# Optimization experiments

Hardware: AMD Instinct MI355X
Metric: run time of the kernel (lower is better)

Reference implementation:

```python
import jax, jax.numpy as jnp
import numpy as np

DIM = 1024
HEADS = 16
HD = DIM // HEADS          # 64
SPECIAL = 8                # CLS/register tokens with full attention
GRID = 32                  # 32x32 patch grid
N = SPECIAL + GRID * GRID  # 1032
B = 8
WINDOW = 3                 # 2D sliding-window radius (7x7 box)
EPS = 1e-6


def _make_2d_mask() -> jnp.ndarray:
    """[N, N] bool mask: special tokens attend everywhere; patches use 2D local box."""
    idx = np.arange(N)
    special = (idx[:, None] < SPECIAL) | (idx[None, :] < SPECIAL)
    p = idx - SPECIAL
    r, c = p // GRID, p % GRID
    swa = (np.abs(r[:, None] - r[None, :]) <= WINDOW) & (np.abs(c[:, None] - c[None, :]) <= WINDOW)
    return jnp.asarray(special | swa)

_MASK = _make_2d_mask()


def setup_inputs() -> dict:
    key = jax.random.key(0)
    k1, k2, k3 = jax.random.split(key, 3)
    hidden_states = jax.random.normal(k1, (B, N, DIM), dtype=jnp.float32)
    qkv_w = jax.random.normal(k2, (3 * DIM, DIM), dtype=jnp.float32) * 0.02
    out_w = jax.random.normal(k3, (DIM, DIM), dtype=jnp.float32) * 0.02
    norm_q_w = jnp.ones((HD,), dtype=jnp.float32)
    norm_k_w = jnp.ones((HD,), dtype=jnp.float32)
    # Standard RoPE tables, half-dim frequencies tiled twice (rotate-half convention)
    pos = np.arange(N, dtype=np.float32)
    inv_freq = 1.0 / (10000.0 ** (np.arange(0, HD, 2, dtype=np.float32) / HD))
    ang = pos[:, None] * inv_freq[None, :]              # [N, HD/2]
    freqs_cos = jnp.asarray(np.concatenate([np.cos(ang), np.cos(ang)], axis=-1))  # [N, HD]
    freqs_sin = jnp.asarray(np.concatenate([np.sin(ang), np.sin(ang)], axis=-1))
    return dict(hidden_states=hidden_states, freqs_cos=freqs_cos, freqs_sin=freqs_sin,
                qkv_w=qkv_w, out_w=out_w, norm_q_w=norm_q_w, norm_k_w=norm_k_w)


def _rms_norm(x, w):
    return x * jax.lax.rsqrt(jnp.mean(x * x, axis=-1, keepdims=True) + EPS) * w


def _rotate_half(x):
    return jnp.concatenate([-x[..., HD // 2:], x[..., :HD // 2]], axis=-1)


def reference(hidden_states, freqs_cos, freqs_sin, qkv_w, out_w, norm_q_w, norm_k_w):
    Bn, Nn, C = hidden_states.shape
    # Fused QKV projection -> [3, B, H, N, D]
    qkv = (hidden_states @ qkv_w.T).reshape(Bn, Nn, 3, HEADS, HD).transpose(2, 0, 3, 1, 4)
    q, k, v = qkv[0], qkv[1], qkv[2]
    # per-head-dim RMSNorm on q, k
    q = _rms_norm(q, norm_q_w)
    k = _rms_norm(k, norm_k_w)
    # RoPE
    cos = freqs_cos[None, None]  # [1,1,N,D]
    sin = freqs_sin[None, None]
    q = q * cos + _rotate_half(q) * sin
    k = k * cos + _rotate_half(k) * sin
    # 2D sliding-window + global-token masked attention
    scale = 1.0 / jnp.sqrt(jnp.asarray(HD, dtype=q.dtype))
    scores = jnp.einsum('bhqd,bhkd->bhqk', q, k) * scale
    neg = jnp.asarray(jnp.finfo(scores.dtype).min, scores.dtype)
    scores = jnp.where(_MASK[None, None], scores, neg)
    probs = jax.nn.softmax(scores, axis=-1)
    attn = jnp.einsum('bhqk,bhkd->bhqd', probs, v)
    attn = attn.transpose(0, 2, 1, 3).reshape(Bn, Nn, C)
    return attn @ out_w.T
```

## Files before the change

### kernel.cpp

```cpp
#include <hip/hip_runtime.h>
#include <hip/hip_bf16.h>

typedef unsigned short ushort_t;
typedef __bf16 bf16x8 __attribute__((ext_vector_type(8)));
typedef float f32x4 __attribute__((ext_vector_type(4)));
typedef float f32x8 __attribute__((ext_vector_type(8)));

#define NTOK 1032
#define NROWS 8256
#define DIMC 1024
#define QKV_ELEMS 8454144
#define XE 8454144
#define QWE 3145728
#define OWE 1048576

__device__ __forceinline__ float bf2f(ushort_t u) {
    union { unsigned int i; float f; } v; v.i = ((unsigned int)u) << 16; return v.f;
}
__device__ __forceinline__ ushort_t f2bf(float f) {
    union { float f; unsigned int i; } v; v.f = f;
    unsigned int r = v.i + 0x7fffu + ((v.i >> 16) & 1u);
    return (ushort_t)(r >> 16);
}
__device__ __forceinline__ bf16x8 cvt8(const float* p) {
    const float4 a = *(const float4*)p;
    const float4 b = *(const float4*)(p + 4);
    bf16x8 r;
    r[0] = (__bf16)a.x; r[1] = (__bf16)a.y; r[2] = (__bf16)a.z; r[3] = (__bf16)a.w;
    r[4] = (__bf16)b.x; r[5] = (__bf16)b.y; r[6] = (__bf16)b.z; r[7] = (__bf16)b.w;
    return r;
}
__device__ __forceinline__ void load_lds16(const ushort_t* g, ushort_t* l) {
    __builtin_amdgcn_global_load_lds(
        (const __attribute__((address_space(1))) unsigned int*)g,
        (__attribute__((address_space(3))) unsigned int*)l, 16, 0, 0);
}

__global__ __launch_bounds__(256) void cvt_kernel(
    const float* __restrict__ X, const float* __restrict__ Wq,
    const float* __restrict__ Wo,
    ushort_t* __restrict__ Xb, ushort_t* __restrict__ Wqb,
    ushort_t* __restrict__ Wob)
{
    const long i8 = ((long)blockIdx.x * 256 + threadIdx.x) * 8;
    const float* src;
    ushort_t* dst;
    long off;
    if (i8 < XE)            { src = X;  dst = Xb;  off = i8; }
    else if (i8 < XE + QWE) { src = Wq; dst = Wqb; off = i8 - XE; }
    else                    { src = Wo; dst = Wob; off = i8 - XE - QWE; }
    *(bf16x8*)(dst + off) = cvt8(src + off);
}

__global__ __launch_bounds__(512, 2) void gemm256_kernel(
    const ushort_t* __restrict__ A, const ushort_t* __restrict__ W,
    ushort_t* __restrict__ QKV)
{
    __shared__ __align__(16) ushort_t A_lds[2 * 16384];
    __shared__ __align__(16) ushort_t B_lds[2 * 16384];

    const int tid  = threadIdx.x;
    const int wave = tid >> 6, lane = tid & 63;
    const int wr = wave >> 2, wc = wave & 3;
    const int fr = lane & 15, quad = lane >> 4;
    const int m0 = blockIdx.y * 256;
    const int n0 = blockIdx.x * 256;
    const bool swap = (blockIdx.x < 8);

    int aoff[4], boff[4];
    #pragma unroll
    for (int ld = 0; ld < 4; ++ld) {
        const int s   = ld * 512 + tid;
        const int row = s >> 3;
        const int kc  = ((s & 7) ^ (row & 7)) * 8;
        int ar = m0 + row; if (ar > NROWS - 1) ar = NROWS - 1;
        aoff[ld] = ar * DIMC + kc;
        boff[ld] = (n0 + row) * DIMC + kc;
    }

    const int ck0 = (quad ^ (fr & 7)) * 8;
    const int ck1 = ((quad + 4) ^ (fr & 7)) * 8;
    const int abase = (wr * 128 + fr) * 64;
    const int bbase = (wc * 64 + fr) * 64;

    f32x4 acc[8][4] = {};

#define SA(ld, t, c) load_lds16(A + aoff[ld] + (t) * 64, \
                                &A_lds[(c) * 16384 + ((ld) * 512 + tid) * 8])
#define SB(ld, t, c) load_lds16(W + boff[ld] + (t) * 64, \
                                &B_lds[(c) * 16384 + ((ld) * 512 + tid) * 8])
#define WAIT_LGKM0 asm volatile("s_waitcnt lgkmcnt(0)" ::: "memory")
#define WAIT_VM6   asm volatile("s_waitcnt vmcnt(6)"  ::: "memory")
#define WAIT_VM0   asm volatile("s_waitcnt vmcnt(0)"  ::: "memory")

    SB(0, 0, 0); SB(1, 0, 0); SB(2, 0, 0); SB(3, 0, 0);
    SA(0, 0, 0); SA(1, 0, 0); SA(2, 0, 0); SA(3, 0, 0);
    SB(0, 1, 1); SB(1, 1, 1); SB(2, 1, 1); SB(3, 1, 1);
    SA(0, 1, 1); SA(2, 1, 1);
    WAIT_VM6;
    __builtin_amdgcn_s_barrier();

    for (int t = 0; t < 16; ++t) {
        const int c = t & 1, o = c ^ 1;
        const int cb = c * 16384;
        bf16x8 bfrag[4][2];
        #pragma unroll
        for (int p = 0; p < 4; ++p) {
            bf16x8 af[2][2];
            #pragma unroll
            for (int mfi = 0; mfi < 2; ++mfi) {
                af[mfi][0] = *(const bf16x8*)&A_lds[cb + abase + (p * 2 + mfi) * 1024 + ck0];
                af[mfi][1] = *(const bf16x8*)&A_lds[cb + abase + (p * 2 + mfi) * 1024 + ck1];
            }
            if (p == 0) {
                #pragma unroll
                for (int nf = 0; nf < 4; ++nf) {
                    bfrag[nf][0] = *(const bf16x8*)&B_lds[cb + bbase + nf * 1024 + ck0];
                    bfrag[nf][1] = *(const bf16x8*)&B_lds[cb + bbase + nf * 1024 + ck1];
                }
                if (t + 1 < 16) { SA(1, t + 1, o); SA(3, t + 1, o); }
            } else if (p == 1) {
                if (t + 2 < 16) { SB(0, t + 2, c); SB(1, t + 2, c);
                                  SB(2, t + 2, c); SB(3, t + 2, c); }
            } else if (p == 2) {
                if (t + 2 < 16) { SA(0, t + 2, c); SA(2, t + 2, c); }
            }
            WAIT_LGKM0;
            if (p < 3) __builtin_amdgcn_s_barrier();
            __builtin_amdgcn_s_setprio(1);
            if (swap) {
                #pragma unroll
                for (int mfi = 0; mfi < 2; ++mfi)
                    #pragma unroll
                    for (int nf = 0; nf < 4; ++nf) {
                        acc[p * 2 + mfi][nf] = __builtin_amdgcn_mfma_f32_16x16x32_bf16(
                            bfrag[nf][0], af[mfi][0], acc[p * 2 + mfi][nf], 0, 0, 0);
                        acc[p * 2 + mfi][nf] = __builtin_amdgcn_mfma_f32_16x16x32_bf16(
                            bfrag[nf][1], af[mfi][1], acc[p * 2 + mfi][nf], 0, 0, 0);
                    }
            } else {
                #pragma unroll
                for (int mfi = 0; mfi < 2; ++mfi)
                    #pragma unroll
                    for (int nf = 0; nf < 4; ++nf) {
                        acc[p * 2 + mfi][nf] = __builtin_amdgcn_mfma_f32_16x16x32_bf16(
                            af[mfi][0], bfrag[nf][0], acc[p * 2 + mfi][nf], 0, 0, 0);
                        acc[p * 2 + mfi][nf] = __builtin_amdgcn_mfma_f32_16x16x32_bf16(
                            af[mfi][1], bfrag[nf][1], acc[p * 2 + mfi][nf], 0, 0, 0);
                    }
            }
            __builtin_amdgcn_s_setprio(0);
        }
        if (t < 14)       { WAIT_VM6; __builtin_amdgcn_s_barrier(); }
        else if (t == 14) { WAIT_VM0; __builtin_amdgcn_s_barrier(); }
    }

    const int rb = quad * 4;
    if (swap) {
        const int part   = n0 >> 10;
        const int hgbase = ((n0 & 1023) + wc * 64) >> 6;
        #pragma unroll
        for (int mf = 0; mf < 8; ++mf) {
            const int m = m0 + wr * 128 + mf * 16 + fr;
            if (m < NROWS) {
                const int bb = m / NTOK, n = m - bb * NTOK;
                ushort_t* outb = QKV + (long)part * QKV_ELEMS +
                    ((long)(bb * 16 + hgbase) * NTOK + n) * 64 + rb;
                #pragma unroll
                for (int nf = 0; nf < 4; ++nf) {
                    ushort4 pk;
                    pk.x = f2bf(acc[mf][nf][0]);
                    pk.y = f2bf(acc[mf][nf][1]);
                    pk.z = f2bf(acc[mf][nf][2]);
                    pk.w = f2bf(acc[mf][nf][3]);
                    *(ushort4*)(outb + nf * 16) = pk;
                }
            }
        }
    } else {
        const int hg = ((n0 & 1023) + wc * 64) >> 6;
        #pragma unroll
        for (int nf = 0; nf < 4; ++nf) {
            const int d = nf * 16 + fr;
            #pragma unroll
            for (int mf = 0; mf < 8; ++mf) {
                const int mb = m0 + wr * 128 + mf * 16 + rb;
                if (mb < NROWS) {
                    const int bb = mb / NTOK, n = mb - bb * NTOK;
                    ushort4 pk;
                    pk.x = f2bf(acc[mf][nf][0]);
                    pk.y = f2bf(acc[mf][nf][1]);
                    pk.z = f2bf(acc[mf][nf][2]);
                    pk.w = f2bf(acc[mf][nf][3]);
                    *(ushort4*)(QKV + 2L * QKV_ELEMS +
                        ((long)((bb * 16 + hg) * 64 + d)) * NTOK + n) = pk;
                }
            }
        }
    }
#undef SA
#undef SB
#undef WAIT_LGKM0
#undef WAIT_VM6
#undef WAIT_VM0
}

template<int MODE>
__global__ __launch_bounds__(256) void gemm_kernel(
    const ushort_t* __restrict__ A, const ushort_t* __restrict__ W,
    ushort_t* __restrict__ QKV, float* __restrict__ Out)
{
    __shared__ __align__(16) ushort_t As0[128 * 32];
    __shared__ __align__(16) ushort_t As1[128 * 32];
    __shared__ __align__(16) ushort_t Bs0[128 * 32];
    __shared__ __align__(16) ushort_t Bs1[128 * 32];
    const int tid  = threadIdx.x;
    const int wave = tid >> 6, lane = tid & 63;
    const int m0 = blockIdx.y * 128;
    const int n0 = blockIdx.x * 128;
    const bool swap = (MODE == 1) || (blockIdx.x < 16);

    f32x4 acc[4][4] = {};

    const int s0 = tid, s1 = tid + 256;
    int ar0 = m0 + (s0 >> 2); if (ar0 > NROWS - 1) ar0 = NROWS - 1;
    int ar1 = m0 + (s1 >> 2); if (ar1 > NROWS - 1) ar1 = NROWS - 1;
    const int br0 = n0 + (s0 >> 2);
    const int br1 = n0 + (s1 >> 2);
    const int kc0 = (s0 & 3) * 8, kc1 = (s1 & 3) * 8;

    const ushort_t* ga0 = A + (long)ar0 * DIMC + kc0;
    const ushort_t* ga1 = A + (long)ar1 * DIMC + kc1;
    const ushort_t* gw0 = W + (long)br0 * DIMC + kc0;
    const ushort_t* gw1 = W + (long)br1 * DIMC + kc1;
    ushort_t* la00 = &As0[s0 * 8]; ushort_t* la01 = &As1[s0 * 8];
    ushort_t* la10 = &As0[s1 * 8]; ushort_t* la11 = &As1[s1 * 8];
    ushort_t* lb00 = &Bs0[s0 * 8]; ushort_t* lb01 = &Bs1[s0 * 8];
    ushort_t* lb10 = &Bs0[s1 * 8]; ushort_t* lb11 = &Bs1[s1 * 8];

    const int wm = (wave >> 1) * 64, wn = (wave & 1) * 64;
    const int fr = lane & 15, fk = (lane >> 4) * 8;
    const int arow = (wm + fr) * 32 + fk;
    const int brow = (wn + fr) * 32 + fk;

    for (int k0 = 0; k0 < DIMC; k0 += 64) {
        load_lds16(ga0 + k0,      la00);
        load_lds16(ga0 + k0 + 32, la01);
        load_lds16(ga1 + k0,      la10);
        load_lds16(ga1 + k0 + 32, la11);
        load_lds16(gw0 + k0,      lb00);
        load_lds16(gw0 + k0 + 32, lb01);
        load_lds16(gw1 + k0,      lb10);
        load_lds16(gw1 + k0 + 32, lb11);
        __syncthreads();

        {
            bf16x8 af[4], bfr[4];
            #pragma unroll
            for (int mi = 0; mi < 4; ++mi)
                af[mi] = *(const bf16x8*)&As0[arow + mi * 16 * 32];
            #pragma unroll
            for (int ni = 0; ni < 4; ++ni)
                bfr[ni] = *(const bf16x8*)&Bs0[brow + ni * 16 * 32];
            if (swap) {
                #pragma unroll
                for (int mi = 0; mi < 4; ++mi)
                    #pragma unroll
                    for (int ni = 0; ni < 4; ++ni)
                        acc[mi][ni] = __builtin_amdgcn_mfma_f32_16x16x32_bf16(
                            bfr[ni], af[mi], acc[mi][ni], 0, 0, 0);
            } else {
                #pragma unroll
                for (int mi = 0; mi < 4; ++mi)
                    #pragma unroll
                    for (int ni = 0; ni < 4; ++ni)
                        acc[mi][ni] = __builtin_amdgcn_mfma_f32_16x16x32_bf16(
                            af[mi], bfr[ni], acc[mi][ni], 0, 0, 0);
            }
        }
        {
            bf16x8 af[4], bfr[4];
            #pragma unroll
            for (int mi = 0; mi < 4; ++mi)
                af[mi] = *(const bf16x8*)&As1[arow + mi * 16 * 32];
            #pragma unroll
            for (int ni = 0; ni < 4; ++ni)
                bfr[ni] = *(const bf16x8*)&Bs1[brow + ni * 16 * 32];
            if (swap) {
                #pragma unroll
                for (int mi = 0; mi < 4; ++mi)
                    #pragma unroll
                    for (int ni = 0; ni < 4; ++ni)
                        acc[mi][ni] = __builtin_amdgcn_mfma_f32_16x16x32_bf16(
                            bfr[ni], af[mi], acc[mi][ni], 0, 0, 0);
            } else {
                #pragma unroll
                for (int mi = 0; mi < 4; ++mi)
                    #pragma unroll
                    for (int ni = 0; ni < 4; ++ni)
                        acc[mi][ni] = __builtin_amdgcn_mfma_f32_16x16x32_bf16(
                            af[mi], bfr[ni], acc[mi][ni], 0, 0, 0);
            }
        }
        __syncthreads();
    }

    const int col = lane & 15, rb = (lane >> 4) * 4;

    if (MODE == 0 && swap) {
        const int part = n0 >> 10;
        #pragma unroll
        for (int mi = 0; mi < 4; ++mi) {
            const int m = m0 + wm + mi * 16 + col;
            if (m < NROWS) {
                const int bb = m / NTOK, n = m - bb * NTOK;
                #pragma unroll
                for (int ni = 0; ni < 4; ++ni) {
                    const int rem = (n0 & 1023) + wn + ni * 16 + rb;
                    const int hg = rem >> 6, d = rem & 63;
                    ushort4 pk;
                    pk.x = f2bf(acc[mi][ni][0]);
                    pk.y = f2bf(acc[mi][ni][1]);
                    pk.z = f2bf(acc[mi][ni][2]);
                    pk.w = f2bf(acc[mi][ni][3]);
                    *(ushort4*)(QKV + (long)part * QKV_ELEMS +
                        ((long)(bb * 16 + hg) * NTOK + n) * 64 + d) = pk;
                }
            }
        }
    } else if (MODE == 0) {
        #pragma unroll
        for (int ni = 0; ni < 4; ++ni) {
            const int o = n0 + wn + ni * 16 + col;
            const int rem = o & 1023;
            const int hg = rem >> 6, d = rem & 63;
            #pragma unroll
            for (int mi = 0; mi < 4; ++mi) {
                const int mb = m0 + wm + mi * 16 + rb;
                if (mb < NROWS) {
                    const int bb = mb / NTOK, n = mb - bb * NTOK;
                    ushort4 pk;
                    pk.x = f2bf(acc[mi][ni][0]);
                    pk.y = f2bf(acc[mi][ni][1]);
                    pk.z = f2bf(acc[mi][ni][2]);
                    pk.w = f2bf(acc[mi][ni][3]);
                    *(ushort4*)(QKV + 2L * QKV_ELEMS +
                        ((long)((bb * 16 + hg) * 64 + d)) * NTOK + n) = pk;
                }
            }
        }
    } else {
        #pragma unroll
        for (int mi = 0; mi < 4; ++mi) {
            const int m = m0 + wm + mi * 16 + col;
            if (m < NROWS) {
                #pragma unroll
                for (int ni = 0; ni < 4; ++ni) {
                    const int o = n0 + wn + ni * 16 + rb;
                    float4 pk;
                    pk.x = acc[mi][ni][0];
                    pk.y = acc[mi][ni][1];
                    pk.z = acc[mi][ni][2];
                    pk.w = acc[mi][ni][3];
                    *(float4*)(Out + (long)m * DIMC + o) = pk;
                }
            }
        }
    }
}

__global__ __launch_bounds__(256) void rope_kernel(
    ushort_t* __restrict__ Qb, ushort_t* __restrict__ Kb,
    const float* __restrict__ cosb, const float* __restrict__ sinb,
    const float* __restrict__ wq, const float* __restrict__ wk)
{
    __shared__ float wsh[64];
    const int idx = blockIdx.x * 256 + threadIdx.x;
    const int tensor = (idx >= 132096) ? 1 : 0;
    const int r = idx - tensor * 132096;
    const int n = r % NTOK;
    if (threadIdx.x < 64) wsh[threadIdx.x] = (tensor ? wk : wq)[threadIdx.x];
    __syncthreads();

    ushort_t* base = (tensor ? Kb : Qb) + (long)r * 64;
    bf16x8 xc[8];
    #pragma unroll
    for (int c = 0; c < 8; ++c) xc[c] = *(const bf16x8*)(base + c * 8);

    float ss = 0.f;
    #pragma unroll
    for (int c = 0; c < 8; ++c) {
        const f32x8 xf = __builtin_convertvector(xc[c], f32x8);
        #pragma unroll
        for (int e = 0; e < 8; ++e) ss += xf[e] * xf[e];
    }
    const float rms = rsqrtf(ss * (1.0f / 64.0f) + 1e-6f);

    const float* cosp = cosb + n * 64;
    const float* sinp = sinb + n * 64;
    #pragma unroll
    for (int c = 0; c < 8; ++c) {
        const f32x8 xf = __builtin_convertvector(xc[c], f32x8);
        const f32x8 pf = __builtin_convertvector(xc[c ^ 4], f32x8);
        const float sgn = (c < 4) ? -1.f : 1.f;
        bf16x8 o8;
        #pragma unroll
        for (int e = 0; e < 8; ++e) {
            const float xn  = xf[e] * rms * wsh[c * 8 + e];
            const float rot = sgn * pf[e] * rms * wsh[(c ^ 4) * 8 + e];
            o8[e] = (__bf16)(xn * cosp[c * 8 + e] + rot * sinp[c * 8 + e]);
        }
        *(bf16x8*)(base + c * 8) = o8;
    }
}

__global__ __launch_bounds__(256) void attn_kernel(
    const ushort_t* __restrict__ Qb, const ushort_t* __restrict__ Kb,
    const ushort_t* __restrict__ Vt, ushort_t* __restrict__ AO)
{
    __shared__ __align__(16) ushort_t KP_s[256 * 72];

    const int tid = threadIdx.x;
    const int wave = tid >> 6, lane = tid & 63;
    const int m_ = lane & 15, quad = lane >> 4;
    const int nb = wave * 64;
    const int d0 = wave * 16;

    bf16x8 ones;
    #pragma unroll
    for (int e = 0; e < 8; ++e) ones[e] = (__bf16)1.0f;

    if (blockIdx.x >= 128) {
        const int blk = blockIdx.x - 128;
        const int bh = blk & 127, qr = blk >> 7;
        const int b = bh >> 4, h = bh & 15;

        int r0 = qr - 3; if (r0 < 0) r0 = 0;
        int r1 = qr + 3; if (r1 > 31) r1 = 31;
        const int limit = 8 + (r1 - r0 + 1) * 32;

        const ushort_t* Qg  = Qb + ((long)bh * NTOK + 8 + qr * 32) * 64;
        const ushort_t* Kg  = Kb + (long)bh * NTOK * 64;
        const ushort_t* Vtg = Vt + (long)bh * 64 * NTOK;

        bf16x8 af[2][2];
        #pragma unroll
        for (int mt = 0; mt < 2; ++mt)
            #pragma unroll
            for (int ks = 0; ks < 2; ++ks)
                af[mt][ks] = *(const bf16x8*)(Qg + (mt * 16 + m_) * 64 + ks * 32 + quad * 8);

        bf16x8 bv[8];
        #pragma unroll
        for (int ks = 0; ks < 8; ++ks) {
            const int slot0 = ks * 32 + quad * 8;
            int tok0;
            if (slot0 >= limit) tok0 = 0;
            else if (slot0 < 8) tok0 = slot0;
            else tok0 = 8 + r0 * 32 + (slot0 - 8);
            bv[ks] = *(const bf16x8*)(Vtg + (long)(d0 + m_) * NTOK + tok0);
        }

        for (int c = tid; c < limit * 8; c += 256) {
            const int slot = c >> 3, c8 = (c & 7) * 8;
            const int tok = slot + (slot >= 8 ? r0 * 32 : 0);
            *(bf16x8*)&KP_s[slot * 72 + c8] = *(const bf16x8*)(Kg + (long)tok * 64 + c8);
        }
        __syncthreads();

        bf16x8 bfr[4][2];
        #pragma unroll
        for (int nt = 0; nt < 4; ++nt)
            #pragma unroll
            for (int ks = 0; ks < 2; ++ks)
                bfr[nt][ks] = *(const bf16x8*)&KP_s[(nb + nt * 16 + m_) * 72 + ks * 32 + quad * 8];

        f32x4 sacc[2][4] = {};
        #pragma unroll
        for (int mt = 0; mt < 2; ++mt)
            #pragma unroll
            for (int nt = 0; nt < 4; ++nt) {
                sacc[mt][nt] = __builtin_amdgcn_mfma_f32_16x16x32_bf16(
                    af[mt][0], bfr[nt][0], sacc[mt][nt], 0, 0, 0);
                sacc[mt][nt] = __builtin_amdgcn_mfma_f32_16x16x32_bf16(
                    af[mt][1], bfr[nt][1], sacc[mt][nt], 0, 0, 0);
            }
        __syncthreads();

        #pragma unroll
        for (int mt = 0; mt < 2; ++mt)
            #pragma unroll
            for (int nt = 0; nt < 4; ++nt) {
                const int slot = nb + nt * 16 + m_;
                const int kc = (slot - 8) & 31;
                #pragma unroll
                for (int reg = 0; reg < 4; ++reg) {
                    const int qm = mt * 16 + quad * 4 + reg;
                    const bool val = (slot < 8) ||
                        ((slot < limit) && ((unsigned)(kc - qm + 3) <= 6u));
                    const float p = val ? __expf(sacc[mt][nt][reg] * 0.125f) : 0.f;
                    KP_s[qm * 280 + slot] = f2bf(p);
                }
            }
        __syncthreads();

        f32x4 oacc[2] = {}, lacc[2] = {};
        #pragma unroll
        for (int ks = 0; ks < 8; ++ks) {
            #pragma unroll
            for (int mt = 0; mt < 2; ++mt) {
                const bf16x8 ap = *(const bf16x8*)&KP_s[(mt * 16 + m_) * 280 + ks * 32 + quad * 8];
                oacc[mt] = __builtin_amdgcn_mfma_f32_16x16x32_bf16(ap, bv[ks], oacc[mt], 0, 0, 0);
                lacc[mt] = __builtin_amdgcn_mfma_f32_16x16x32_bf16(ap, ones,   lacc[mt], 0, 0, 0);
            }
        }
        #pragma unroll
        for (int mt = 0; mt < 2; ++mt)
            #pragma unroll
            for (int reg = 0; reg < 4; ++reg) {
                const int qm = mt * 16 + quad * 4 + reg;
                const int tok = 8 + qr * 32 + qm;
                AO[((long)(b * NTOK + tok)) * DIMC + h * 64 + d0 + m_] =
                    f2bf(oacc[mt][reg] / lacc[mt][reg]);
            }
    } else {
        const int bh = blockIdx.x;
        const int b = bh >> 4, h = bh & 15;
        const ushort_t* Kg  = Kb + (long)bh * NTOK * 64;
        const ushort_t* Vtg = Vt + (long)bh * 64 * NTOK;

        bf16x8 afs[2];
        if (m_ < 8) {
            #pragma unroll
            for (int ks = 0; ks < 2; ++ks)
                afs[ks] = *(const bf16x8*)(Qb + ((long)bh * NTOK + m_) * 64 + ks * 32 + quad * 8);
        } else {
            #pragma unroll
            for (int ks = 0; ks < 2; ++ks)
                #pragma unroll
                for (int e = 0; e < 8; ++e) afs[ks][e] = (__bf16)0.f;
        }

        f32x4 oacc = {}, lacc = {};
        for (int ch = 0; ch < 5; ++ch) {
            const int tok0 = ch * 256;
            const int limit = (NTOK - tok0 < 256) ? (NTOK - tok0) : 256;

            bf16x8 bv[8];
            #pragma unroll
            for (int ks = 0; ks < 8; ++ks) {
                const int slot0 = ks * 32 + quad * 8;
                const int tok = tok0 + ((slot0 < limit) ? slot0 : 0);
                bv[ks] = *(const bf16x8*)(Vtg + (long)(d0 + m_) * NTOK + tok);
            }

            __syncthreads();
            for (int c = tid; c < limit * 8; c += 256) {
                const int slot = c >> 3, c8 = (c & 7) * 8;
                *(bf16x8*)&KP_s[slot * 72 + c8] =
                    *(const bf16x8*)(Kg + (long)(tok0 + slot) * 64 + c8);
            }
            __syncthreads();

            bf16x8 bfr[4][2];
            #pragma unroll
            for (int nt = 0; nt < 4; ++nt)
                #pragma unroll
                for (int ks = 0; ks < 2; ++ks)
                    bfr[nt][ks] = *(const bf16x8*)&KP_s[(nb + nt * 16 + m_) * 72 + ks * 32 + quad * 8];
            f32x4 sacc[4] = {};
            #pragma unroll
            for (int nt = 0; nt < 4; ++nt) {
                sacc[nt] = __builtin_amdgcn_mfma_f32_16x16x32_bf16(afs[0], bfr[nt][0], sacc[nt], 0, 0, 0);
                sacc[nt] = __builtin_amdgcn_mfma_f32_16x16x32_bf16(afs[1], bfr[nt][1], sacc[nt], 0, 0, 0);
            }
            __syncthreads();

            #pragma unroll
            for (int nt = 0; nt < 4; ++nt) {
                const int slot = nb + nt * 16 + m_;
                const bool val = (slot < limit);
                #pragma unroll
                for (int reg = 0; reg < 4; ++reg) {
                    const int qm = quad * 4 + reg;
                    const float p = val ? __expf(sacc[nt][reg] * 0.125f) : 0.f;
                    KP_s[qm * 280 + slot] = f2bf(p);
                }
            }
            __syncthreads();

            #pragma unroll
            for (int ks = 0; ks < 8; ++ks) {
                const bf16x8 ap = *(const bf16x8*)&KP_s[m_ * 280 + ks * 32 + quad * 8];
                oacc = __builtin_amdgcn_mfma_f32_16x16x32_bf16(ap, bv[ks], oacc, 0, 0, 0);
                lacc = __builtin_amdgcn_mfma_f32_16x16x32_bf16(ap, ones,   lacc, 0, 0, 0);
            }
        }

        #pragma unroll
        for (int reg = 0; reg < 4; ++reg) {
            const int qm = quad * 4 + reg;
            if (qm < 8) {
                AO[((long)(b * NTOK + qm)) * DIMC + h * 64 + d0 + m_] =
                    f2bf(oacc[reg] / lacc[reg]);
            }
        }
    }
}

extern "C" void kernel_launch(void* const* d_in, const int* in_sizes, int n_in,
                              void* d_out, int out_size, void* d_ws, size_t ws_size,
                              hipStream_t stream) {
    const float* X    = (const float*)d_in[0];
    const float* fc   = (const float*)d_in[1];
    const float* fs   = (const float*)d_in[2];
    const float* qkvw = (const float*)d_in[3];
    const float* outw = (const float*)d_in[4];
    const float* nqw  = (const float*)d_in[5];
    const float* nkw  = (const float*)d_in[6];

    ushort_t* Qb  = (ushort_t*)d_ws;
    ushort_t* Kb  = Qb + QKV_ELEMS;
    ushort_t* Vt  = Kb + QKV_ELEMS;
    ushort_t* AO  = Vt + QKV_ELEMS;
    ushort_t* Xb  = AO + QKV_ELEMS;
    ushort_t* Wqb = Xb + XE;
    ushort_t* Wob = Wqb + QWE;
    float* Out = (float*)d_out;

    cvt_kernel<<<6176, 256, 0, stream>>>(X, qkvw, outw, Xb, Wqb, Wob);
    gemm256_kernel<<<dim3(12, 33), 512, 0, stream>>>(Xb, Wqb, Qb);
    rope_kernel<<<1032, 256, 0, stream>>>(Qb, Kb, fc, fs, nqw, nkw);
    attn_kernel<<<4224, 256, 0, stream>>>(Qb, Kb, Vt, AO);
    gemm_kernel<1><<<dim3(8, 65), 256, 0, stream>>>(AO, Wob, nullptr, Out);
}
```

Measured before the change: 305.2 us.

## Use 256x256 pipelined GEMM for output projection and restructure phase barriers

Templates the 256x256 tiled, double-buffered GEMM so it also serves the output projection, writing fp32 output, and removes the older 128x128 GEMM. Separately, it rewrites the main loop into explicit phases: each phase issues LDS reads and global prefetches, then a barrier and a sched_barrier, then the MFMA block. The larger tiles give more data reuse, but the output GEMM now launches only 132 blocks, which may underfill the GPU. The extra barriers may also add synchronisation cost.

```diff
diff --git a/kernel.cpp b/kernel.cpp
--- a/kernel.cpp
+++ b/kernel.cpp
@@ -52,9 +52,10 @@
     *(bf16x8*)(dst + off) = cvt8(src + off);
 }
 
+template<int MODE>
 __global__ __launch_bounds__(512, 2) void gemm256_kernel(
     const ushort_t* __restrict__ A, const ushort_t* __restrict__ W,
-    ushort_t* __restrict__ QKV)
+    ushort_t* __restrict__ QKV, float* __restrict__ Out)
 {
     __shared__ __align__(16) ushort_t A_lds[2 * 16384];
     __shared__ __align__(16) ushort_t B_lds[2 * 16384];
@@ -65,7 +66,7 @@
     const int fr = lane & 15, quad = lane >> 4;
     const int m0 = blockIdx.y * 256;
     const int n0 = blockIdx.x * 256;
-    const bool swap = (blockIdx.x < 8);
+    const bool swap = (MODE == 1) || (blockIdx.x < 8);
 
     int aoff[4], boff[4];
     #pragma unroll
@@ -93,6 +94,37 @@
 #define WAIT_VM6   asm volatile("s_waitcnt vmcnt(6)"  ::: "memory")
 #define WAIT_VM0   asm volatile("s_waitcnt vmcnt(0)"  ::: "memory")
 
+#define READ_AF(p) \
+    af[0][0] = *(const bf16x8*)&A_lds[cb + abase + ((p) * 2 + 0) * 1024 + ck0]; \
+    af[0][1] = *(const bf16x8*)&A_lds[cb + abase + ((p) * 2 + 0) * 1024 + ck1]; \
+    af[1][0] = *(const bf16x8*)&A_lds[cb + abase + ((p) * 2 + 1) * 1024 + ck0]; \
+    af[1][1] = *(const bf16x8*)&A_lds[cb + abase + ((p) * 2 + 1) * 1024 + ck1];
+
+#define MFMA_PHASE(p) \
+    __builtin_amdgcn_s_setprio(1); \
+    if (swap) { \
+        _Pragma("unroll") \
+        for (int mfi = 0; mfi < 2; ++mfi) \
+            _Pragma("unroll") \
+            for (int nf = 0; nf < 4; ++nf) { \
+                acc[(p) * 2 + mfi][nf] = __builtin_amdgcn_mfma_f32_16x16x32_bf16( \
+                    bfrag[nf][0], af[mfi][0], acc[(p) * 2 + mfi][nf], 0, 0, 0); \
+                acc[(p) * 2 + mfi][nf] = __builtin_amdgcn_mfma_f32_16x16x32_bf16( \
+                    bfrag[nf][1], af[mfi][1], acc[(p) * 2 + mfi][nf], 0, 0, 0); \
+            } \
+    } else { \
+        _Pragma("unroll") \
+        for (int mfi = 0; mfi < 2; ++mfi) \
+            _Pragma("unroll") \
+            for (int nf = 0; nf < 4; ++nf) { \
+                acc[(p) * 2 + mfi][nf] = __builtin_amdgcn_mfma_f32_16x16x32_bf16( \
+                    af[mfi][0], bfrag[nf][0], acc[(p) * 2 + mfi][nf], 0, 0, 0); \
+                acc[(p) * 2 + mfi][nf] = __builtin_amdgcn_mfma_f32_16x16x32_bf16( \
+                    af[mfi][1], bfrag[nf][1], acc[(p) * 2 + mfi][nf], 0, 0, 0); \
+            } \
+    } \
+    __builtin_amdgcn_s_setprio(0);
+
     SB(0, 0, 0); SB(1, 0, 0); SB(2, 0, 0); SB(3, 0, 0);
     SA(0, 0, 0); SA(1, 0, 0); SA(2, 0, 0); SA(3, 0, 0);
     SB(0, 1, 1); SB(1, 1, 1); SB(2, 1, 1); SB(3, 1, 1);
@@ -104,59 +136,62 @@
         const int c = t & 1, o = c ^ 1;
         const int cb = c * 16384;
         bf16x8 bfrag[4][2];
-        #pragma unroll
-        for (int p = 0; p < 4; ++p) {
-            bf16x8 af[2][2];
-            #pragma unroll
-            for (int mfi = 0; mfi < 2; ++mfi) {
-                af[mfi][0] = *(const bf16x8*)&A_lds[cb + abase + (p * 2 + mfi) * 1024 + ck0];
-                af[mfi][1] = *(const bf16x8*)&A_lds[cb + abase + (p * 2 + mfi) * 1024 + ck1];
-            }
-            if (p == 0) {
-                #pragma unroll
-                for (int nf = 0; nf < 4; ++nf) {
-                    bfrag[nf][0] = *(const bf16x8*)&B_lds[cb + bbase + nf * 1024 + ck0];
-                    bfrag[nf][1] = *(const bf16x8*)&B_lds[cb + bbase + nf * 1024 + ck1];
-                }
-                if (t + 1 < 16) { SA(1, t + 1, o); SA(3, t + 1, o); }
-            } else if (p == 1) {
-                if (t + 2 < 16) { SB(0, t + 2, c); SB(1, t + 2, c);
-                                  SB(2, t + 2, c); SB(3, t + 2, c); }
-            } else if (p == 2) {
-                if (t + 2 < 16) { SA(0, t + 2, c); SA(2, t + 2, c); }
-            }
-            WAIT_LGKM0;
-            if (p < 3) __builtin_amdgcn_s_barrier();
-            __builtin_amdgcn_s_setprio(1);
-            if (swap) {
-                #pragma unroll
-                for (int mfi = 0; mfi < 2; ++mfi)
-                    #pragma unroll
-                    for (int nf = 0; nf < 4; ++nf) {
-                        acc[p * 2 + mfi][nf] = __builtin_amdgcn_mfma_f32_16x16x32_bf16(
-                            bfrag[nf][0], af[mfi][0], acc[p * 2 + mfi][nf], 0, 0, 0);
-                        acc[p * 2 + mfi][nf] = __builtin_amdgcn_mfma_f32_16x16x32_bf16(
-                            bfrag[nf][1], af[mfi][1], acc[p * 2 + mfi][nf], 0, 0, 0);
-                    }
-            } else {
-                #pragma unroll
-                for (int mfi = 0; mfi < 2; ++mfi)
-                    #pragma unroll
-                    for (int nf = 0; nf < 4; ++nf) {
-                        acc[p * 2 + mfi][nf] = __builtin_amdgcn_mfma_f32_16x16x32_bf16(
-                            af[mfi][0], bfrag[nf][0], acc[p * 2 + mfi][nf], 0, 0, 0);
-                        acc[p * 2 + mfi][nf] = __builtin_amdgcn_mfma_f32_16x16x32_bf16(
-                            af[mfi][1], bfrag[nf][1], acc[p * 2 + mfi][nf], 0, 0, 0);
-                    }
-            }
-            __builtin_amdgcn_s_setprio(0);
-        }
+        bf16x8 af[2][2];
+
+        #pragma unroll
+        for (int nf = 0; nf < 4; ++nf) {
+            bfrag[nf][0] = *(const bf16x8*)&B_lds[cb + bbase + nf * 1024 + ck0];
+            bfrag[nf][1] = *(const bf16x8*)&B_lds[cb + bbase + nf * 1024 + ck1];
+        }
+        READ_AF(0);
+        if (t < 15) { SA(1, t + 1, o); SA(3, t + 1, o); }
+        __builtin_amdgcn_s_barrier();
+        WAIT_LGKM0; __builtin_amdgcn_sched_barrier(0);
+        MFMA_PHASE(0);
+        __builtin_amdgcn_s_barrier();
+
+        READ_AF(1);
+        if (t < 14) { SB(0, t + 2, c); SB(1, t + 2, c);
+                      SB(2, t + 2, c); SB(3, t + 2, c); }
+        __builtin_amdgcn_s_barrier();
+        WAIT_LGKM0; __builtin_amdgcn_sched_barrier(0);
+        MFMA_PHASE(1);
+        __builtin_amdgcn_s_barrier();
+
+        READ_AF(2);
+        if (t < 14) { SA(0, t + 2, c); SA(2, t + 2, c); }
+        __builtin_amdgcn_s_barrier();
+        WAIT_LGKM0; __builtin_amdgcn_sched_barrier(0);
+        MFMA_PHASE(2);
+
+        READ_AF(3);
+        __builtin_amdgcn_s_barrier();
+        WAIT_LGKM0; __builtin_amdgcn_sched_barrier(0);
+        MFMA_PHASE(3);
+
         if (t < 14)       { WAIT_VM6; __builtin_amdgcn_s_barrier(); }
         else if (t == 14) { WAIT_VM0; __builtin_amdgcn_s_barrier(); }
     }
 
     const int rb = quad * 4;
-    if (swap) {
+    if (MODE == 1) {
+        #pragma unroll
+        for (int mf = 0; mf < 8; ++mf) {
+            const int m = m0 + wr * 128 + mf * 16 + fr;
+            if (m < NROWS) {
+                #pragma unroll
+                for (int nf = 0; nf < 4; ++nf) {
+                    const int o_ = n0 + wc * 64 + nf * 16 + rb;
+                    float4 pk;
+                    pk.x = acc[mf][nf][0];
+                    pk.y = acc[mf][nf][1];
+                    pk.z = acc[mf][nf][2];
+                    pk.w = acc[mf][nf][3];
+                    *(float4*)(Out + (long)m * DIMC + o_) = pk;
+                }
+            }
+        }
+    } else if (swap) {
         const int part   = n0 >> 10;
         const int hgbase = ((n0 & 1023) + wc * 64) >> 6;
         #pragma unroll
@@ -203,170 +238,8 @@
 #undef WAIT_LGKM0
 #undef WAIT_VM6
 #undef WAIT_VM0
-}
-
-template<int MODE>
-__global__ __launch_bounds__(256) void gemm_kernel(
-    const ushort_t* __restrict__ A, const ushort_t* __restrict__ W,
-    ushort_t* __restrict__ QKV, float* __restrict__ Out)
-{
-    __shared__ __align__(16) ushort_t As0[128 * 32];
-    __shared__ __align__(16) ushort_t As1[128 * 32];
-    __shared__ __align__(16) ushort_t Bs0[128 * 32];
-    __shared__ __align__(16) ushort_t Bs1[128 * 32];
-    const int tid  = threadIdx.x;
-    const int wave = tid >> 6, lane = tid & 63;
-    const int m0 = blockIdx.y * 128;
-    const int n0 = blockIdx.x * 128;
-    const bool swap = (MODE == 1) || (blockIdx.x < 16);
-
-    f32x4 acc[4][4] = {};
-
-    const int s0 = tid, s1 = tid + 256;
-    int ar0 = m0 + (s0 >> 2); if (ar0 > NROWS - 1) ar0 = NROWS - 1;
-    int ar1 = m0 + (s1 >> 2); if (ar1 > NROWS - 1) ar1 = NROWS - 1;
-    const int br0 = n0 + (s0 >> 2);
-    const int br1 = n0 + (s1 >> 2);
-    const int kc0 = (s0 & 3) * 8, kc1 = (s1 & 3) * 8;
-
-    const ushort_t* ga0 = A + (long)ar0 * DIMC + kc0;
-    const ushort_t* ga1 = A + (long)ar1 * DIMC + kc1;
-    const ushort_t* gw0 = W + (long)br0 * DIMC + kc0;
-    const ushort_t* gw1 = W + (long)br1 * DIMC + kc1;
-    ushort_t* la00 = &As0[s0 * 8]; ushort_t* la01 = &As1[s0 * 8];
-    ushort_t* la10 = &As0[s1 * 8]; ushort_t* la11 = &As1[s1 * 8];
-    ushort_t* lb00 = &Bs0[s0 * 8]; ushort_t* lb01 = &Bs1[s0 * 8];
-    ushort_t* lb10 = &Bs0[s1 * 8]; ushort_t* lb11 = &Bs1[s1 * 8];
-
-    const int wm = (wave >> 1) * 64, wn = (wave & 1) * 64;
-    const int fr = lane & 15, fk = (lane >> 4) * 8;
-    const int arow = (wm + fr) * 32 + fk;
-    const int brow = (wn + fr) * 32 + fk;
-
-    for (int k0 = 0; k0 < DIMC; k0 += 64) {
-        load_lds16(ga0 + k0,      la00);
-        load_lds16(ga0 + k0 + 32, la01);
-        load_lds16(ga1 + k0,      la10);
-        load_lds16(ga1 + k0 + 32, la11);
-        load_lds16(gw0 + k0,      lb00);
-        load_lds16(gw0 + k0 + 32, lb01);
-        load_lds16(gw1 + k0,      lb10);
-        load_lds16(gw1 + k0 + 32, lb11);
-        __syncthreads();
-
-        {
-            bf16x8 af[4], bfr[4];
-            #pragma unroll
-            for (int mi = 0; mi < 4; ++mi)
-                af[mi] = *(const bf16x8*)&As0[arow + mi * 16 * 32];
-            #pragma unroll
-            for (int ni = 0; ni < 4; ++ni)
-                bfr[ni] = *(const bf16x8*)&Bs0[brow + ni * 16 * 32];
-            if (swap) {
-                #pragma unroll
-                for (int mi = 0; mi < 4; ++mi)
-                    #pragma unroll
-                    for (int ni = 0; ni < 4; ++ni)
-                        acc[mi][ni] = __builtin_amdgcn_mfma_f32_16x16x32_bf16(
-                            bfr[ni], af[mi], acc[mi][ni], 0, 0, 0);
-            } else {
-                #pragma unroll
-                for (int mi = 0; mi < 4; ++mi)
-                    #pragma unroll
-                    for (int ni = 0; ni < 4; ++ni)
-                        acc[mi][ni] = __builtin_amdgcn_mfma_f32_16x16x32_bf16(
-                            af[mi], bfr[ni], acc[mi][ni], 0, 0, 0);
-            }
-        }
-        {
-            bf16x8 af[4], bfr[4];
-            #pragma unroll
-            for (int mi = 0; mi < 4; ++mi)
-                af[mi] = *(const bf16x8*)&As1[arow + mi * 16 * 32];
-            #pragma unroll
-            for (int ni = 0; ni < 4; ++ni)
-                bfr[ni] = *(const bf16x8*)&Bs1[brow + ni * 16 * 32];
-            if (swap) {
-                #pragma unroll
-                for (int mi = 0; mi < 4; ++mi)
-                    #pragma unroll
-                    for (int ni = 0; ni < 4; ++ni)
-                        acc[mi][ni] = __builtin_amdgcn_mfma_f32_16x16x32_bf16(
-                            bfr[ni], af[mi], acc[mi][ni], 0, 0, 0);
-            } else {
-                #pragma unroll
-                for (int mi = 0; mi < 4; ++mi)
-                    #pragma unroll
-                    for (int ni = 0; ni < 4; ++ni)
-                        acc[mi][ni] = __builtin_amdgcn_mfma_f32_16x16x32_bf16(
-                            af[mi], bfr[ni], acc[mi][ni], 0, 0, 0);
-            }
-        }
-        __syncthreads();
-    }
-
-    const int col = lane & 15, rb = (lane >> 4) * 4;
-
-    if (MODE == 0 && swap) {
-        const int part = n0 >> 10;
-        #pragma unroll
-        for (int mi = 0; mi < 4; ++mi) {
-            const int m = m0 + wm + mi * 16 + col;
-            if (m < NROWS) {
-                const int bb = m / NTOK, n = m - bb * NTOK;
-                #pragma unroll
-                for (int ni = 0; ni < 4; ++ni) {
-                    const int rem = (n0 & 1023) + wn + ni * 16 + rb;
-                    const int hg = rem >> 6, d = rem & 63;
-                    ushort4 pk;
-                    pk.x = f2bf(acc[mi][ni][0]);
-                    pk.y = f2bf(acc[mi][ni][1]);
-                    pk.z = f2bf(acc[mi][ni][2]);
-                    pk.w = f2bf(acc[mi][ni][3]);
-                    *(ushort4*)(QKV + (long)part * QKV_ELEMS +
-                        ((long)(bb * 16 + hg) * NTOK + n) * 64 + d) = pk;
-                }
-            }
-        }
-    } else if (MODE == 0) {
-        #pragma unroll
-        for (int ni = 0; ni < 4; ++ni) {
-            const int o = n0 + wn + ni * 16 + col;
-            const int rem = o & 1023;
-            const int hg = rem >> 6, d = rem & 63;
-            #pragma unroll
-            for (int mi = 0; mi < 4; ++mi) {
-                const int mb = m0 + wm + mi * 16 + rb;
-                if (mb < NROWS) {
-                    const int bb = mb / NTOK, n = mb - bb * NTOK;
-                    ushort4 pk;
-                    pk.x = f2bf(acc[mi][ni][0]);
-                    pk.y = f2bf(acc[mi][ni][1]);
-                    pk.z = f2bf(acc[mi][ni][2]);
-                    pk.w = f2bf(acc[mi][ni][3]);
-                    *(ushort4*)(QKV + 2L * QKV_ELEMS +
-                        ((long)((bb * 16 + hg) * 64 + d)) * NTOK + n) = pk;
-                }
-            }
-        }
-    } else {
-        #pragma unroll
-        for (int mi = 0; mi < 4; ++mi) {
-            const int m = m0 + wm + mi * 16 + col;
-            if (m < NROWS) {
-                #pragma unroll
-                for (int ni = 0; ni < 4; ++ni) {
-                    const int o = n0 + wn + ni * 16 + rb;
-                    float4 pk;
-                    pk.x = acc[mi][ni][0];
-                    pk.y = acc[mi][ni][1];
-                    pk.z = acc[mi][ni][2];
-                    pk.w = acc[mi][ni][3];
-                    *(float4*)(Out + (long)m * DIMC + o) = pk;
-                }
-            }
-        }
-    }
+#undef READ_AF
+#undef MFMA_PHASE
 }
 
 __global__ __launch_bounds__(256) void rope_kernel(
@@ -629,8 +502,8 @@
     float* Out = (float*)d_out;
 
     cvt_kernel<<<6176, 256, 0, stream>>>(X, qkvw, outw, Xb, Wqb, Wob);
-    gemm256_kernel<<<dim3(12, 33), 512, 0, stream>>>(Xb, Wqb, Qb);
+    gemm256_kernel<0><<<dim3(12, 33), 512, 0, stream>>>(Xb, Wqb, Qb, nullptr);
     rope_kernel<<<1032, 256, 0, stream>>>(Qb, Kb, fc, fs, nqw, nkw);
     attn_kernel<<<4224, 256, 0, stream>>>(Qb, Kb, Vt, AO);
-    gemm_kernel<1><<<dim3(8, 65), 256, 0, stream>>>(AO, Wob, nullptr, Out);
-}
+    gemm256_kernel<1><<<dim3(4, 33), 512, 0, stream>>>(AO, Wob, nullptr, Out);
+}
```

New measurement: 309.6 us. No clear change (+1.4%).
